# Kernel tuning notes

Measured on AMD Instinct MI355X. Metric: run time of the kernel, lower is better.

Reference implementation:

```python
import jax, jax.numpy as jnp
import numpy as np

N_HEAD = 16
ROPE_BASE = 10000.0


def rope_cos_sin(T, head_dim, dtype):
    inv_freq = 1.0 / (ROPE_BASE ** (jnp.arange(0, head_dim, 2, dtype=jnp.float32) / head_dim))
    t = jnp.arange(T, dtype=jnp.float32)
    freqs = jnp.einsum('i,j->ij', t, inv_freq)          # [T, head_dim/2]
    emb = jnp.concatenate([freqs, freqs], axis=-1)       # [T, head_dim]
    return jnp.cos(emb).astype(dtype), jnp.sin(emb).astype(dtype)


def rotate_half(x):
    h = x.shape[-1] // 2
    return jnp.concatenate([-x[..., h:], x[..., :h]], axis=-1)


def setup_inputs() -> dict:
    key = jax.random.key(0)
    ks = jax.random.split(key, 5)
    B, T, C = 2, 1024, 2048
    s = 0.02
    return {
        'x': jax.random.normal(ks[0], (B, T, C), dtype=jnp.float32),
        'Wq': jax.random.normal(ks[1], (C, C), dtype=jnp.float32) * s,
        'Wk': jax.random.normal(ks[2], (C, C), dtype=jnp.float32) * s,
        'Wv': jax.random.normal(ks[3], (C, C), dtype=jnp.float32) * s,
        'Wo': jax.random.normal(ks[4], (C, C), dtype=jnp.float32) * s,
    }


def reference(x, Wq, Wk, Wv, Wo):
    B, T, C = x.shape
    H = N_HEAD
    D = C // H
    # torch Linear: y = x @ W.T  (W is [out, in])
    q = jnp.einsum('btc,oc->bto', x, Wq).reshape(B, T, H, D).transpose(0, 2, 1, 3)
    k = jnp.einsum('btc,oc->bto', x, Wk).reshape(B, T, H, D).transpose(0, 2, 1, 3)
    v = jnp.einsum('btc,oc->bto', x, Wv).reshape(B, T, H, D).transpose(0, 2, 1, 3)
    cos, sin = rope_cos_sin(T, D, x.dtype)               # [T, D]
    cos = cos[None, None]                                 # [1,1,T,D]
    sin = sin[None, None]
    q = q * cos + rotate_half(q) * sin
    k = k * cos + rotate_half(k) * sin
    scale = 1.0 / jnp.sqrt(jnp.asarray(D, dtype=x.dtype))
    att = jnp.einsum('bhqd,bhkd->bhqk', q, k) * scale    # [B,H,T,T]
    causal = jnp.tril(jnp.ones((T, T), dtype=bool))
    att = jnp.where(causal[None, None], att, jnp.finfo(x.dtype).min)
    att = jax.nn.softmax(att, axis=-1)
    y = jnp.einsum('bhqk,bhkd->bhqd', att, v)            # [B,H,T,D]
    y = y.transpose(0, 2, 1, 3).reshape(B, T, C)
    return jnp.einsum('btc,oc->bto', y, Wo)
```

## Files before the change

kernel.cpp:

```cpp
#include <hip/hip_runtime.h>
#include <stdint.h>

typedef unsigned short u16;
typedef __bf16 bf16x8 __attribute__((ext_vector_type(8)));
typedef float  f32x4  __attribute__((ext_vector_type(4)));

#define B_  2
#define T_  1024
#define C_  2048
#define H_  16
#define D_  128
#define NTENS 4194304

__device__ __forceinline__ u16 f2bf(float f) {
    union { float f; uint32_t u; } v; v.f = f;
    uint32_t r = (v.u + 0x7FFFu + ((v.u >> 16) & 1u)) >> 16;
    return (u16)r;
}
__device__ __forceinline__ float bf2f(u16 h) {
    union { uint32_t u; float f; } v; v.u = ((uint32_t)h) << 16;
    return v.f;
}
__device__ __forceinline__ float fexp2(float x) {
    return __builtin_amdgcn_exp2f(x);
}

__global__ __launch_bounds__(256) void k_convert(
    const float* __restrict__ x, const float* __restrict__ wq,
    const float* __restrict__ wk, const float* __restrict__ wv,
    const float* __restrict__ wo, u16* __restrict__ dst,
    float* __restrict__ ct, float* __restrict__ st)
{
    int z = blockIdx.z;
    if (z == 5) {
        int idx = blockIdx.x * 256 + threadIdx.x;
        if (idx < 65536) {
            int t = idx >> 6, d = idx & 63;
            float inv = expf(-(float)d * (9.210340371976184f / 64.0f));
            float th = (float)t * inv;
            float s, c;
            sincosf(th, &s, &c);
            ct[idx] = c;
            st[idx] = s;
        }
        return;
    }
    const float* src = (z == 0) ? x : (z == 1) ? wq : (z == 2) ? wk : (z == 3) ? wv : wo;
    u16* d = dst + (size_t)z * NTENS;
    size_t i = ((size_t)blockIdx.x * 256 + threadIdx.x) * 4;
    float4 v = *(const float4*)(src + i);
    ushort4 o;
    o.x = f2bf(v.x); o.y = f2bf(v.y); o.z = f2bf(v.z); o.w = f2bf(v.w);
    *(ushort4*)(d + i) = o;
}

template<int MTILE, int EPI>
__device__ __forceinline__ void gemm_tile_nt(
    const u16* __restrict__ A, int lda,
    const u16* __restrict__ Bp, int ldb,
    void* __restrict__ Cp, int ldc,
    int m0, int n0, int K,
    u16* SMEM, const float* __restrict__ ct, const float* __restrict__ st, int z)
{
    constexpr int MF  = MTILE / 16;
    constexpr int ACH = MTILE / 32;
    u16* As = SMEM;
    u16* Bs = SMEM + MTILE * 64;

    const int tid  = threadIdx.x;
    const int wave = tid >> 6;
    const int lane = tid & 63;
    const int frow = lane & 15;
    const int quad = lane >> 4;

    const int lrow8  = lane >> 3;
    const int slot   = lane & 7;
    const int gchunk = slot ^ lrow8;

    f32x4 acc[MF][2] = {};

    size_t aoff[ACH], boff[4];
#pragma unroll
    for (int i = 0; i < ACH; ++i) {
        int c = (i << 2) + wave;
        int r = (c << 3) + lrow8;
        aoff[i] = (size_t)(m0 + r) * lda + (gchunk << 3);
    }
#pragma unroll
    for (int i = 0; i < 4; ++i) {
        int r = (i << 5) + (wave << 3) + lrow8;
        boff[i] = (size_t)(n0 + r) * ldb + (gchunk << 3);
    }

    for (int kt = 0; kt < K; kt += 64) {
#pragma unroll
        for (int i = 0; i < ACH; ++i) {
            int c = (i << 2) + wave;
            __builtin_amdgcn_global_load_lds(
                (const __attribute__((address_space(1))) void*)(A + aoff[i] + kt),
                (__attribute__((address_space(3))) void*)(As + (c << 9)), 16, 0, 0);
        }
#pragma unroll
        for (int i = 0; i < 4; ++i) {
            int c = (i << 2) + wave;
            __builtin_amdgcn_global_load_lds(
                (const __attribute__((address_space(1))) void*)(Bp + boff[i] + kt),
                (__attribute__((address_space(3))) void*)(Bs + (c << 9)), 16, 0, 0);
        }
        __syncthreads();

#pragma unroll
        for (int ks = 0; ks < 2; ++ks) {
            int lk = (ks << 2) + quad;
            bf16x8 af[MF], bfv[2];
#pragma unroll
            for (int i = 0; i < MF; ++i) {
                int ar = (i << 4) + frow;
                af[i] = *(const bf16x8*)&As[ar * 64 + ((lk ^ (frow & 7)) << 3)];
            }
#pragma unroll
            for (int j = 0; j < 2; ++j) {
                int br = (wave << 4) + (j << 6) + frow;
                bfv[j] = *(const bf16x8*)&Bs[br * 64 + ((lk ^ (frow & 7)) << 3)];
            }
#pragma unroll
            for (int i = 0; i < MF; ++i)
#pragma unroll
                for (int j = 0; j < 2; ++j)
                    acc[i][j] = __builtin_amdgcn_mfma_f32_16x16x32_bf16(
                        af[i], bfv[j], acc[i][j], 0, 0, 0);
        }
        __syncthreads();
    }

    if constexpr (EPI == 2) {
        if (z < 2) {
            const int d = (wave << 4) + frow;
            const float sc = (z == 0) ? 0.12751743368f : 1.0f;
            u16* Op = (u16*)Cp;
#pragma unroll
            for (int i = 0; i < MF; ++i)
#pragma unroll
                for (int r = 0; r < 4; ++r) {
                    int m = m0 + (i << 4) + (quad << 2) + r;
                    int t = m & 1023;
                    float c = ct[t * 64 + d], s = st[t * 64 + d];
                    float a = acc[i][0][r], bb = acc[i][1][r];
                    Op[(size_t)m * ldc + n0 + d]      = f2bf((a * c - bb * s) * sc);
                    Op[(size_t)m * ldc + n0 + d + 64] = f2bf((bb * c + a * s) * sc);
                }
            return;
        }
        const int hh = n0 >> 7;
        const int bI = m0 >> 10;
        const int t0 = m0 & 1023;
        u16* Vp = (u16*)Cp + ((size_t)((bI << 4) + hh)) * (D_ * T_);
#pragma unroll
        for (int i = 0; i < MF; ++i)
#pragma unroll
            for (int j = 0; j < 2; ++j) {
                int d = (wave << 4) + (j << 6) + frow;
                int t = t0 + (i << 4) + (quad << 2);
                ushort4 o;
                o.x = f2bf(acc[i][j][0]); o.y = f2bf(acc[i][j][1]);
                o.z = f2bf(acc[i][j][2]); o.w = f2bf(acc[i][j][3]);
                *(ushort4*)&Vp[(size_t)d * T_ + t] = o;
            }
        return;
    }

#pragma unroll
    for (int i = 0; i < MF; ++i)
#pragma unroll
        for (int j = 0; j < 2; ++j)
#pragma unroll
            for (int r = 0; r < 4; ++r) {
                int m = m0 + (i << 4) + (quad << 2) + r;
                int n = n0 + (wave << 4) + (j << 6) + frow;
                if constexpr (EPI == 0)
                    ((float*)Cp)[(size_t)m * ldc + n] = acc[i][j][r];
                else
                    ((u16*)Cp)[(size_t)m * ldc + n] = f2bf(acc[i][j][r]);
            }
}

__global__ __launch_bounds__(256) void k_gemm_qkv(
    const u16* __restrict__ xb, const u16* __restrict__ wq,
    const u16* __restrict__ wk, const u16* __restrict__ wv,
    u16* __restrict__ q, u16* __restrict__ k, u16* __restrict__ vt,
    const float* __restrict__ ct, const float* __restrict__ st)
{
    __shared__ u16 SMEM[64 * 64 + 128 * 64];
    int z = blockIdx.z;
    const u16* Bp = (z == 0) ? wq : (z == 1) ? wk : wv;
    u16* Op       = (z == 0) ? q  : (z == 1) ? k  : vt;
    gemm_tile_nt<64, 2>(xb, C_, Bp, C_, Op, C_,
                        blockIdx.y * 64, blockIdx.x * 128, C_, SMEM, ct, st, z);
}

__global__ __launch_bounds__(256) void k_flash(
    const u16* __restrict__ qb, const u16* __restrict__ kb,
    const u16* __restrict__ vt, u16* __restrict__ yb)
{
    __shared__ u16 Ks[128 * 128];
    __shared__ u16 Vs[128 * 128];

    const int bx  = blockIdx.x;
    const int bh  = bx & 31, b = bh >> 4, h = bh & 15;
    const int qt  = (bx < 256) ? (15 - (bx >> 5)) : ((bx >> 5) - 8);
    const int KT  = (qt >> 1) + 1;
    const int tid = threadIdx.x, wave = tid >> 6, lane = tid & 63;
    const int frow = lane & 15, quad = lane >> 4;

    const u16* qbase = qb + (size_t)b * (T_ * C_) + h * D_;
    const u16* kbase = kb + (size_t)b * (T_ * C_) + h * D_;
    const u16* vbase = vt + (size_t)bh * (D_ * T_);
    const int q0 = qt << 6;

    bf16x8 qf[4];
#pragma unroll
    for (int ks = 0; ks < 4; ++ks)
        qf[ks] = *(const bf16x8*)&qbase[(size_t)(q0 + (wave << 4) + frow) * C_
                                        + (ks << 5) + (quad << 3)];

    f32x4 Y[8] = {};
    float mrow[4], lrow[4];
#pragma unroll
    for (int r = 0; r < 4; ++r) { mrow[r] = -3e38f; lrow[r] = 0.f; }

    const int tok = q0 + (wave << 4) + (quad << 2);

    for (int kt = 0; kt < KT; ++kt) {
        const int k0 = kt << 7;
        {
            const int r4 = lane >> 4, s16 = lane & 15;
#pragma unroll
            for (int i = 0; i < 8; ++i) {
                int c = (i << 2) + wave;
                int row = (c << 2) + r4;
                int g = (s16 & 8) | ((s16 & 7) ^ (row & 7));
                __builtin_amdgcn_global_load_lds(
                    (const __attribute__((address_space(1))) void*)(kbase + (size_t)(k0 + row) * C_ + (g << 3)),
                    (__attribute__((address_space(3))) void*)(Ks + (c << 9)), 16, 0, 0);
            }
#pragma unroll
            for (int i = 0; i < 8; ++i) {
                int c = (i << 2) + wave;
                int row = (c << 2) + r4;
                int g = (s16 & 8) | ((s16 & 7) ^ (row & 7));
                __builtin_amdgcn_global_load_lds(
                    (const __attribute__((address_space(1))) void*)(vbase + (size_t)row * T_ + k0 + (g << 3)),
                    (__attribute__((address_space(3))) void*)(Vs + (c << 9)), 16, 0, 0);
            }
        }
        asm volatile("s_waitcnt vmcnt(8)" ::: "memory");
        __builtin_amdgcn_sched_barrier(0);
        __builtin_amdgcn_s_barrier();
        __builtin_amdgcn_sched_barrier(0);

        f32x4 S[8] = {};
#pragma unroll
        for (int ks = 0; ks < 4; ++ks) {
            int lk = (ks << 2) + quad;
            int sw = ((lk & 8) | ((lk & 7) ^ (frow & 7))) << 3;
#pragma unroll
            for (int jj = 0; jj < 8; ++jj) {
                bf16x8 bb = *(const bf16x8*)&Ks[((jj << 4) + frow) * 128 + sw];
                S[jj] = __builtin_amdgcn_mfma_f32_16x16x32_bf16(qf[ks], bb, S[jj], 0, 0, 0);
            }
        }

        if (kt == KT - 1) {
#pragma unroll
            for (int jj = 0; jj < 8; ++jj) {
                int colg = k0 + (jj << 4) + frow;
#pragma unroll
                for (int r = 0; r < 4; ++r)
                    if (colg > tok + r) S[jj][r] = -1e30f;
            }
        }

        float al[4];
#pragma unroll
        for (int r = 0; r < 4; ++r) {
            float tm = -3e38f;
#pragma unroll
            for (int jj = 0; jj < 8; ++jj) tm = fmaxf(tm, S[jj][r]);
#pragma unroll
            for (int off = 8; off > 0; off >>= 1) tm = fmaxf(tm, __shfl_xor(tm, off));
            float mn = fmaxf(mrow[r], tm);
            al[r] = fexp2(mrow[r] - mn);
            mrow[r] = mn;
            float rs = 0.f;
#pragma unroll
            for (int jj = 0; jj < 8; ++jj) {
                float e = fexp2(S[jj][r] - mn);
                S[jj][r] = e;
                rs += e;
            }
#pragma unroll
            for (int off = 8; off > 0; off >>= 1) rs += __shfl_xor(rs, off);
            lrow[r] = lrow[r] * al[r] + rs;
        }
#pragma unroll
        for (int dj = 0; dj < 8; ++dj)
#pragma unroll
            for (int r = 0; r < 4; ++r) Y[dj][r] *= al[r];

        __syncthreads();

        u16* Ps = Ks;
#pragma unroll
        for (int jj = 0; jj < 8; ++jj)
#pragma unroll
            for (int r = 0; r < 4; ++r)
                Ps[((wave << 4) + (quad << 2) + r) * 136 + (jj << 4) + frow] = f2bf(S[jj][r]);

#pragma unroll
        for (int ks = 0; ks < 4; ++ks) {
            bf16x8 pa = *(const bf16x8*)&Ps[((wave << 4) + frow) * 136 + (ks << 5) + (quad << 3)];
            int lk = (ks << 2) + quad;
            int sw = ((lk & 8) | ((lk & 7) ^ (frow & 7))) << 3;
#pragma unroll
            for (int dj = 0; dj < 8; ++dj) {
                bf16x8 vv = *(const bf16x8*)&Vs[((dj << 4) + frow) * 128 + sw];
                Y[dj] = __builtin_amdgcn_mfma_f32_16x16x32_bf16(pa, vv, Y[dj], 0, 0, 0);
            }
        }
        __syncthreads();
    }

    u16* ybase = yb + (size_t)b * (T_ * C_) + h * D_;
#pragma unroll
    for (int r = 0; r < 4; ++r) {
        float inv = 1.0f / lrow[r];
#pragma unroll
        for (int dj = 0; dj < 8; ++dj)
            ybase[(size_t)(tok + r) * C_ + (dj << 4) + frow] = f2bf(Y[dj][r] * inv);
    }
}

__global__ __launch_bounds__(256) void k_gemm_out(
    const u16* __restrict__ yb, const u16* __restrict__ wo, float* __restrict__ out)
{
    __shared__ u16 SMEM[64 * 64 + 128 * 64];
    gemm_tile_nt<64, 0>(yb, C_, wo, C_, out, C_,
                        blockIdx.y * 64, blockIdx.x * 128, C_, SMEM, nullptr, nullptr, 0);
}

extern "C" void kernel_launch(void* const* d_in, const int* in_sizes, int n_in,
                              void* d_out, int out_size, void* d_ws, size_t ws_size,
                              hipStream_t stream)
{
    (void)in_sizes; (void)n_in; (void)out_size; (void)ws_size;
    const float* x  = (const float*)d_in[0];
    const float* Wq = (const float*)d_in[1];
    const float* Wk = (const float*)d_in[2];
    const float* Wv = (const float*)d_in[3];
    const float* Wo = (const float*)d_in[4];

    u16* ws  = (u16*)d_ws;
    u16* xb  = ws;
    u16* wqb = ws + (size_t)1 * NTENS;
    u16* wkb = ws + (size_t)2 * NTENS;
    u16* wvb = ws + (size_t)3 * NTENS;
    u16* wob = ws + (size_t)4 * NTENS;
    u16* qb  = ws + (size_t)5 * NTENS;
    u16* kb  = ws + (size_t)6 * NTENS;
    u16* yb  = ws + (size_t)8 * NTENS;
    u16* vt  = ws + (size_t)9 * NTENS;
    float* ct = (float*)(ws + (size_t)10 * NTENS);
    float* st = ct + 65536;

    k_convert <<<dim3(4096, 1, 6), 256, 0, stream>>>(x, Wq, Wk, Wv, Wo, ws, ct, st);
    k_gemm_qkv<<<dim3(16, 32, 3), 256, 0, stream>>>(xb, wqb, wkb, wvb, qb, kb, vt, ct, st);
    k_flash   <<<dim3(512), 256, 0, stream>>>(qb, kb, vt, yb);
    k_gemm_out<<<dim3(16, 32, 1), 256, 0, stream>>>(yb, wob, (float*)d_out);
}
```

Baseline: 239.5 us.

## Prefetch next K/V tiles in flash attention and give P its own swizzled buffer

The flash-attention kernel now gives the probability tile P its own XOR-swizzled shared buffer instead of reusing the K buffer. This lets the next K tile be loaded asynchronously while P·V runs, and the next V tile be loaded after P·V finishes, overlapping global loads with compute. The added LDS per block (16 KB) can lower occupancy. The vmcnt(8) wait placement must still match the split issue order of the K and V loads.

```diff
diff --git a/kernel.cpp b/kernel.cpp
--- a/kernel.cpp
+++ b/kernel.cpp
@@ -204,6 +204,7 @@
 {
     __shared__ u16 Ks[128 * 128];
     __shared__ u16 Vs[128 * 128];
+    __shared__ u16 Ps[64 * 128];
 
     const int bx  = blockIdx.x;
     const int bh  = bx & 31, b = bh >> 4, h = bh & 15;
@@ -229,32 +230,39 @@
     for (int r = 0; r < 4; ++r) { mrow[r] = -3e38f; lrow[r] = 0.f; }
 
     const int tok = q0 + (wave << 4) + (quad << 2);
+    const int r4 = lane >> 4, s16 = lane & 15;
+
+    auto stageK = [&](int k0) {
+#pragma unroll
+        for (int i = 0; i < 8; ++i) {
+            int c = (i << 2) + wave;
+            int row = (c << 2) + r4;
+            int g = (s16 & 8) | ((s16 & 7) ^ (row & 7));
+            __builtin_amdgcn_global_load_lds(
+                (const __attribute__((address_space(1))) void*)(kbase + (size_t)(k0 + row) * C_ + (g << 3)),
+                (__attribute__((address_space(3))) void*)(Ks + (c << 9)), 16, 0, 0);
+        }
+    };
+    auto stageV = [&](int k0) {
+#pragma unroll
+        for (int i = 0; i < 8; ++i) {
+            int c = (i << 2) + wave;
+            int row = (c << 2) + r4;
+            int g = (s16 & 8) | ((s16 & 7) ^ (row & 7));
+            __builtin_amdgcn_global_load_lds(
+                (const __attribute__((address_space(1))) void*)(vbase + (size_t)row * T_ + k0 + (g << 3)),
+                (__attribute__((address_space(3))) void*)(Vs + (c << 9)), 16, 0, 0);
+        }
+    };
+
+    stageK(0);
+    stageV(0);
 
     for (int kt = 0; kt < KT; ++kt) {
         const int k0 = kt << 7;
-        {
-            const int r4 = lane >> 4, s16 = lane & 15;
-#pragma unroll
-            for (int i = 0; i < 8; ++i) {
-                int c = (i << 2) + wave;
-                int row = (c << 2) + r4;
-                int g = (s16 & 8) | ((s16 & 7) ^ (row & 7));
-                __builtin_amdgcn_global_load_lds(
-                    (const __attribute__((address_space(1))) void*)(kbase + (size_t)(k0 + row) * C_ + (g << 3)),
-                    (__attribute__((address_space(3))) void*)(Ks + (c << 9)), 16, 0, 0);
-            }
-#pragma unroll
-            for (int i = 0; i < 8; ++i) {
-                int c = (i << 2) + wave;
-                int row = (c << 2) + r4;
-                int g = (s16 & 8) | ((s16 & 7) ^ (row & 7));
-                __builtin_amdgcn_global_load_lds(
-                    (const __attribute__((address_space(1))) void*)(vbase + (size_t)row * T_ + k0 + (g << 3)),
-                    (__attribute__((address_space(3))) void*)(Vs + (c << 9)), 16, 0, 0);
-            }
-        }
+
+        __builtin_amdgcn_sched_barrier(0);
         asm volatile("s_waitcnt vmcnt(8)" ::: "memory");
-        __builtin_amdgcn_sched_barrier(0);
         __builtin_amdgcn_s_barrier();
         __builtin_amdgcn_sched_barrier(0);
 
@@ -307,18 +315,31 @@
 #pragma unroll
             for (int r = 0; r < 4; ++r) Y[dj][r] *= al[r];
 
-        __syncthreads();
-
-        u16* Ps = Ks;
 #pragma unroll
         for (int jj = 0; jj < 8; ++jj)
 #pragma unroll
-            for (int r = 0; r < 4; ++r)
-                Ps[((wave << 4) + (quad << 2) + r) * 136 + (jj << 4) + frow] = f2bf(S[jj][r]);
+            for (int r = 0; r < 4; ++r) {
+                int prow = (wave << 4) + (quad << 2) + r;
+                int pcol = (jj << 4) + frow;
+                Ps[prow * 128 + ((((pcol >> 3) ^ (prow & 7)) << 3) | (frow & 7))]
+                    = f2bf(S[jj][r]);
+            }
+
+        __builtin_amdgcn_sched_barrier(0);
+        asm volatile("s_waitcnt vmcnt(0)" ::: "memory");
+        __builtin_amdgcn_s_barrier();
+        __builtin_amdgcn_sched_barrier(0);
+
+        if (kt + 1 < KT) {
+            stageK(k0 + 128);
+            __builtin_amdgcn_sched_barrier(0);
+        }
 
 #pragma unroll
         for (int ks = 0; ks < 4; ++ks) {
-            bf16x8 pa = *(const bf16x8*)&Ps[((wave << 4) + frow) * 136 + (ks << 5) + (quad << 3)];
+            int pch = (ks << 2) + quad;
+            bf16x8 pa = *(const bf16x8*)&Ps[((wave << 4) + frow) * 128
+                                            + ((pch ^ (frow & 7)) << 3)];
             int lk = (ks << 2) + quad;
             int sw = ((lk & 8) | ((lk & 7) ^ (frow & 7))) << 3;
 #pragma unroll
@@ -327,7 +348,15 @@
                 Y[dj] = __builtin_amdgcn_mfma_f32_16x16x32_bf16(pa, vv, Y[dj], 0, 0, 0);
             }
         }
-        __syncthreads();
+
+        __builtin_amdgcn_sched_barrier(0);
+        __builtin_amdgcn_s_barrier();
+        __builtin_amdgcn_sched_barrier(0);
+
+        if (kt + 1 < KT) {
+            stageV(k0 + 128);
+            __builtin_amdgcn_sched_barrier(0);
+        }
     }
 
     u16* ybase = yb + (size_t)b * (T_ * C_) + h * D_;
```

Measured after the change: 243.0 us. No clear change (+1.5%).

## Have each flash-attention wave process two query row-tiles to reuse K/V fragments

Applied to the files above, without the earlier changes.

The flash kernel now runs 2 waves of 128 threads instead of 4, and each wave handles 32 query rows (two 16-row MFMA tiles). Every K and V fragment read from LDS then feeds two MFMAs, halving LDS read traffic per MFMA. The trade-off is about twice the accumulator and Q registers per wave, fewer waves per block to hide latency, and twice as many async loads per thread. The vmcnt wait is updated to match the new load count.

```diff
diff --git a/kernel.cpp b/kernel.cpp
--- a/kernel.cpp
+++ b/kernel.cpp
@@ -198,7 +198,7 @@
                         blockIdx.y * 64, blockIdx.x * 128, C_, SMEM, ct, st, z);
 }
 
-__global__ __launch_bounds__(256) void k_flash(
+__global__ __launch_bounds__(128) void k_flash(
     const u16* __restrict__ qb, const u16* __restrict__ kb,
     const u16* __restrict__ vt, u16* __restrict__ yb)
 {
@@ -217,26 +217,31 @@
     const u16* vbase = vt + (size_t)bh * (D_ * T_);
     const int q0 = qt << 6;
 
-    bf16x8 qf[4];
-#pragma unroll
-    for (int ks = 0; ks < 4; ++ks)
-        qf[ks] = *(const bf16x8*)&qbase[(size_t)(q0 + (wave << 4) + frow) * C_
-                                        + (ks << 5) + (quad << 3)];
-
-    f32x4 Y[8] = {};
-    float mrow[4], lrow[4];
-#pragma unroll
-    for (int r = 0; r < 4; ++r) { mrow[r] = -3e38f; lrow[r] = 0.f; }
-
-    const int tok = q0 + (wave << 4) + (quad << 2);
+    bf16x8 qf[2][4];
+#pragma unroll
+    for (int m = 0; m < 2; ++m)
+#pragma unroll
+        for (int ks = 0; ks < 4; ++ks)
+            qf[m][ks] = *(const bf16x8*)&qbase[
+                (size_t)(q0 + (wave << 5) + (m << 4) + frow) * C_
+                + (ks << 5) + (quad << 3)];
+
+    f32x4 Y[2][8] = {};
+    float mrow[2][4], lrow[2][4];
+#pragma unroll
+    for (int m = 0; m < 2; ++m)
+#pragma unroll
+        for (int r = 0; r < 4; ++r) { mrow[m][r] = -3e38f; lrow[m][r] = 0.f; }
+
+    const int tokw = q0 + (wave << 5) + (quad << 2);
 
     for (int kt = 0; kt < KT; ++kt) {
         const int k0 = kt << 7;
         {
             const int r4 = lane >> 4, s16 = lane & 15;
 #pragma unroll
-            for (int i = 0; i < 8; ++i) {
-                int c = (i << 2) + wave;
+            for (int i = 0; i < 16; ++i) {
+                int c = (i << 1) + wave;
                 int row = (c << 2) + r4;
                 int g = (s16 & 8) | ((s16 & 7) ^ (row & 7));
                 __builtin_amdgcn_global_load_lds(
@@ -244,8 +249,8 @@
                     (__attribute__((address_space(3))) void*)(Ks + (c << 9)), 16, 0, 0);
             }
 #pragma unroll
-            for (int i = 0; i < 8; ++i) {
-                int c = (i << 2) + wave;
+            for (int i = 0; i < 16; ++i) {
+                int c = (i << 1) + wave;
                 int row = (c << 2) + r4;
                 int g = (s16 & 8) | ((s16 & 7) ^ (row & 7));
                 __builtin_amdgcn_global_load_lds(
@@ -253,12 +258,12 @@
                     (__attribute__((address_space(3))) void*)(Vs + (c << 9)), 16, 0, 0);
             }
         }
-        asm volatile("s_waitcnt vmcnt(8)" ::: "memory");
+        asm volatile("s_waitcnt vmcnt(16)" ::: "memory");
         __builtin_amdgcn_sched_barrier(0);
         __builtin_amdgcn_s_barrier();
         __builtin_amdgcn_sched_barrier(0);
 
-        f32x4 S[8] = {};
+        f32x4 S[2][8] = {};
 #pragma unroll
         for (int ks = 0; ks < 4; ++ks) {
             int lk = (ks << 2) + quad;
@@ -266,65 +271,79 @@
 #pragma unroll
             for (int jj = 0; jj < 8; ++jj) {
                 bf16x8 bb = *(const bf16x8*)&Ks[((jj << 4) + frow) * 128 + sw];
-                S[jj] = __builtin_amdgcn_mfma_f32_16x16x32_bf16(qf[ks], bb, S[jj], 0, 0, 0);
+                S[0][jj] = __builtin_amdgcn_mfma_f32_16x16x32_bf16(qf[0][ks], bb, S[0][jj], 0, 0, 0);
+                S[1][jj] = __builtin_amdgcn_mfma_f32_16x16x32_bf16(qf[1][ks], bb, S[1][jj], 0, 0, 0);
             }
         }
 
         if (kt == KT - 1) {
 #pragma unroll
-            for (int jj = 0; jj < 8; ++jj) {
-                int colg = k0 + (jj << 4) + frow;
+            for (int m = 0; m < 2; ++m)
+#pragma unroll
+                for (int jj = 0; jj < 8; ++jj) {
+                    int colg = k0 + (jj << 4) + frow;
+#pragma unroll
+                    for (int r = 0; r < 4; ++r)
+                        if (colg > tokw + (m << 4) + r) S[m][jj][r] = -1e30f;
+                }
+        }
+
+        float al[2][4];
+#pragma unroll
+        for (int m = 0; m < 2; ++m)
+#pragma unroll
+            for (int r = 0; r < 4; ++r) {
+                float tm = -3e38f;
+#pragma unroll
+                for (int jj = 0; jj < 8; ++jj) tm = fmaxf(tm, S[m][jj][r]);
+#pragma unroll
+                for (int off = 8; off > 0; off >>= 1) tm = fmaxf(tm, __shfl_xor(tm, off));
+                float mn = fmaxf(mrow[m][r], tm);
+                al[m][r] = fexp2(mrow[m][r] - mn);
+                mrow[m][r] = mn;
+                float rs = 0.f;
+#pragma unroll
+                for (int jj = 0; jj < 8; ++jj) {
+                    float e = fexp2(S[m][jj][r] - mn);
+                    S[m][jj][r] = e;
+                    rs += e;
+                }
+#pragma unroll
+                for (int off = 8; off > 0; off >>= 1) rs += __shfl_xor(rs, off);
+                lrow[m][r] = lrow[m][r] * al[m][r] + rs;
+            }
+#pragma unroll
+        for (int m = 0; m < 2; ++m)
+#pragma unroll
+            for (int dj = 0; dj < 8; ++dj)
+#pragma unroll
+                for (int r = 0; r < 4; ++r) Y[m][dj][r] *= al[m][r];
+
+        __syncthreads();
+
+        u16* Ps = Ks;
+#pragma unroll
+        for (int m = 0; m < 2; ++m)
+#pragma unroll
+            for (int jj = 0; jj < 8; ++jj)
 #pragma unroll
                 for (int r = 0; r < 4; ++r)
-                    if (colg > tok + r) S[jj][r] = -1e30f;
-            }
-        }
-
-        float al[4];
-#pragma unroll
-        for (int r = 0; r < 4; ++r) {
-            float tm = -3e38f;
-#pragma unroll
-            for (int jj = 0; jj < 8; ++jj) tm = fmaxf(tm, S[jj][r]);
-#pragma unroll
-            for (int off = 8; off > 0; off >>= 1) tm = fmaxf(tm, __shfl_xor(tm, off));
-            float mn = fmaxf(mrow[r], tm);
-            al[r] = fexp2(mrow[r] - mn);
-            mrow[r] = mn;
-            float rs = 0.f;
-#pragma unroll
-            for (int jj = 0; jj < 8; ++jj) {
-                float e = fexp2(S[jj][r] - mn);
-                S[jj][r] = e;
-                rs += e;
-            }
-#pragma unroll
-            for (int off = 8; off > 0; off >>= 1) rs += __shfl_xor(rs, off);
-            lrow[r] = lrow[r] * al[r] + rs;
-        }
-#pragma unroll
-        for (int dj = 0; dj < 8; ++dj)
-#pragma unroll
-            for (int r = 0; r < 4; ++r) Y[dj][r] *= al[r];
-
-        __syncthreads();
-
-        u16* Ps = Ks;
-#pragma unroll
-        for (int jj = 0; jj < 8; ++jj)
-#pragma unroll
-            for (int r = 0; r < 4; ++r)
-                Ps[((wave << 4) + (quad << 2) + r) * 136 + (jj << 4) + frow] = f2bf(S[jj][r]);
+                    Ps[((wave << 5) + (m << 4) + (quad << 2) + r) * 136
+                       + (jj << 4) + frow] = f2bf(S[m][jj][r]);
 
 #pragma unroll
         for (int ks = 0; ks < 4; ++ks) {
-            bf16x8 pa = *(const bf16x8*)&Ps[((wave << 4) + frow) * 136 + (ks << 5) + (quad << 3)];
+            bf16x8 pa0 = *(const bf16x8*)&Ps[((wave << 5) + frow) * 136
+                                             + (ks << 5) + (quad << 3)];
+            bf16x8 pa1 = *(const bf16x8*)&Ps[((wave << 5) + 16 + frow) * 136
+                                             + (ks << 5) + (quad << 3)];
             int lk = (ks << 2) + quad;
             int sw = ((lk & 8) | ((lk & 7) ^ (frow & 7))) << 3;
 #pragma unroll
             for (int dj = 0; dj < 8; ++dj) {
                 bf16x8 vv = *(const bf16x8*)&Vs[((dj << 4) + frow) * 128 + sw];
-                Y[dj] = __builtin_amdgcn_mfma_f32_16x16x32_bf16(pa, vv, Y[dj], 0, 0, 0);
+                Y[0][dj] = __builtin_amdgcn_mfma_f32_16x16x32_bf16(pa0, vv, Y[0][dj], 0, 0, 0);
+                Y[1][dj] = __builtin_amdgcn_mfma_f32_16x16x32_bf16(pa1, vv, Y[1][dj], 0, 0, 0);
             }
         }
         __syncthreads();
@@ -332,12 +351,15 @@
 
     u16* ybase = yb + (size_t)b * (T_ * C_) + h * D_;
 #pragma unroll
-    for (int r = 0; r < 4; ++r) {
-        float inv = 1.0f / lrow[r];
-#pragma unroll
-        for (int dj = 0; dj < 8; ++dj)
-            ybase[(size_t)(tok + r) * C_ + (dj << 4) + frow] = f2bf(Y[dj][r] * inv);
-    }
+    for (int m = 0; m < 2; ++m)
+#pragma unroll
+        for (int r = 0; r < 4; ++r) {
+            float inv = 1.0f / lrow[m][r];
+#pragma unroll
+            for (int dj = 0; dj < 8; ++dj)
+                ybase[(size_t)(tokw + (m << 4) + r) * C_ + (dj << 4) + frow]
+                    = f2bf(Y[m][dj][r] * inv);
+        }
 }
 
 __global__ __launch_bounds__(256) void k_gemm_out(
@@ -374,6 +396,6 @@
 
     k_convert <<<dim3(4096, 1, 6), 256, 0, stream>>>(x, Wq, Wk, Wv, Wo, ws, ct, st);
     k_gemm_qkv<<<dim3(16, 32, 3), 256, 0, stream>>>(xb, wqb, wkb, wvb, qb, kb, vt, ct, st);
-    k_flash   <<<dim3(512), 256, 0, stream>>>(qb, kb, vt, yb);
+    k_flash   <<<dim3(512), 128, 0, stream>>>(qb, kb, vt, yb);
     k_gemm_out<<<dim3(16, 32, 1), 256, 0, stream>>>(yb, wob, (float*)d_out);
 }
```

New measurement: 263.3 us. +9.9%, slower.
